# Optimization experiments

Measured on AMD Instinct MI355X. Metric: run time of the kernel, lower is better.

## Reference

```python
import jax, jax.numpy as jnp
import numpy as np

INPUT_SIZE = 256
HIDDEN_SIZE = 1024
NUM_LAYERS = 2
BATCH = 16
SEQ_LEN = 2048
K = 10
JI0 = 0.4
JII = -0.1


def setup_inputs() -> dict:
    key = jax.random.key(0)
    kx, kih, khh, kow, kob = jax.random.split(key, 5)
    x = jax.random.normal(kx, (BATCH, SEQ_LEN, INPUT_SIZE), dtype=jnp.float32)
    # sparse balanced-network init: each entry nonzero with prob K/fan_in, value J/sqrt(K)
    mih = jax.random.bernoulli(kih, K / INPUT_SIZE, (NUM_LAYERS, HIDDEN_SIZE, INPUT_SIZE))
    weight_ih = mih.astype(jnp.float32) * (JI0 / np.sqrt(K))
    mhh = jax.random.bernoulli(khh, K / HIDDEN_SIZE, (NUM_LAYERS, HIDDEN_SIZE, HIDDEN_SIZE))
    weight_hh = mhh.astype(jnp.float32) * (JII / np.sqrt(K))
    out_w = jax.random.normal(kow, (INPUT_SIZE, HIDDEN_SIZE), dtype=jnp.float32) / np.sqrt(HIDDEN_SIZE)
    out_b = jax.random.normal(kob, (INPUT_SIZE,), dtype=jnp.float32) * 0.01
    return {"x": x, "weight_ih": weight_ih, "weight_hh": weight_hh, "out_w": out_w, "out_b": out_b}


def reference(x, weight_ih, weight_hh, out_w, out_b):
    L = weight_hh.shape[0]
    H = weight_hh.shape[1]
    B = x.shape[0]
    c = jnp.sqrt(jnp.asarray(K, dtype=x.dtype))  # const_ff_input (broadcast scalar)
    xs = jnp.transpose(x, (1, 0, 2))  # [S, B, I]  (batch_first -> time major)
    h0 = jnp.zeros((L, B, H), dtype=x.dtype)

    def step(h_prev, x_t):
        hs = []
        for l in range(L):
            if l == 0:
                ff = x_t @ weight_ih[0].T
            else:
                # NOTE: original code uses weight_hh (not weight_ih) for deep-layer ff input
                ff = hs[l - 1] @ weight_hh[l].T
            hs.append(jax.nn.relu(c + ff + h_prev[l] @ weight_hh[l].T))
        h = jnp.stack(hs)  # [L, B, H]
        return h, hs[-1]

    h_T, outs = jax.lax.scan(step, h0, xs)  # outs: [S, B, H]
    out = jnp.transpose(outs, (1, 0, 2)) @ out_w.T + out_b  # [B, S, I]
    return out, h_T
```

## Files before the change

kernel.cpp:

```cpp
#include <hip/hip_runtime.h>
#include <hip/hip_bf16.h>
#include <cstddef>

#define BATCH 16
#define SEQ   2048
#define ISZ   256
#define H     1024
#define CAPE  56
#define MAXDEG 40
#define CAP0  48
#define CAP1  32
#define HP    1056
#define SENTX 256

static __device__ __forceinline__ float bf2f(unsigned short u) {
    unsigned v = ((unsigned)u) << 16;
    float f; __builtin_memcpy(&f, &v, 4); return f;
}


__global__ void init_kernel(unsigned short* eih, unsigned short* e0r, unsigned short* e1r,
                            unsigned short* e0b, unsigned short* e1b,
                            int* cih, int* c0, int* c1, int* sih, int* s0, int* s1,
                            int* nw, float* jv) {
    int t = blockIdx.x * blockDim.x + threadIdx.x;
    if (t < CAPE * H) { eih[t] = SENTX; e0r[t] = 1024; e1r[t] = 1024; e0b[t] = 1024; e1b[t] = 1024; }
    if (t < H) { cih[t] = 0; c0[t] = 0; c1[t] = 0; sih[t] = 0; s0[t] = 0; s1[t] = 0; }
    if (t < 32) nw[t] = 0;
    if (t < 4) jv[t] = 0.f;
}

__global__ void count_ih(const float* __restrict__ wih, int* cih, float* jv) {
    int t = blockIdx.x * blockDim.x + threadIdx.x;
    float w = wih[t];
    if (w != 0.f) { atomicAdd(&cih[t >> 8], 1); jv[0] = w; }
}

__global__ void count_hh(const float* __restrict__ whh, int* c0, int* c1, float* jv) {
    int t = blockIdx.x * blockDim.x + threadIdx.x;
    float w = whh[t];
    if (w != 0.f) {
        int l = t >> 20, j = (t >> 10) & 1023;
        if (l == 0) { atomicAdd(&c0[j], 1); jv[1] = w; }
        else        { atomicAdd(&c1[j], 1); jv[2] = w; }
    }
}

__global__ __launch_bounds__(1024) void sortperm(const int* __restrict__ c0, const int* __restrict__ c1,
                                                 int* p0, int* ip0, int* p1, int* ip1) {
    const int* c = blockIdx.x ? c1 : c0;
    int* p  = blockIdx.x ? p1  : p0;
    int* ip = blockIdx.x ? ip1 : ip0;
    __shared__ int hist[CAPE + 1];
    __shared__ int base[CAPE + 1];
    int j = threadIdx.x;
    if (j <= CAPE) hist[j] = 0;
    __syncthreads();
    int cv = min(c[j], CAPE);
    atomicAdd(&hist[cv], 1);
    __syncthreads();
    if (j == 0) { int acc = 0; for (int k = 0; k <= CAPE; ++k) { base[k] = acc; acc += hist[k]; } }
    __syncthreads();
    int pos = atomicAdd(&base[cv], 1);
    p[pos] = j;
    ip[j] = pos;
}

__global__ void build_ih(const float* __restrict__ wih, const int* __restrict__ ip0,
                         unsigned short* eih, int* sih) {
    int t = blockIdx.x * blockDim.x + threadIdx.x;
    if (wih[t] != 0.f) {
        int j = t >> 8, i = t & 255;
        int r = ip0[j];
        int s = atomicAdd(&sih[r], 1);
        if (s < CAPE) eih[(s >> 1) * (2 * H) + r * 2 + (s & 1)] = (unsigned short)i;
    }
}

__global__ void build_hh(const float* __restrict__ whh, const int* __restrict__ ip0,
                         const int* __restrict__ ip1,
                         unsigned short* e0r, unsigned short* e1r, int* s0, int* s1) {
    int t = blockIdx.x * blockDim.x + threadIdx.x;
    float w = whh[t];
    if (w != 0.f) {
        int l = t >> 20, j = (t >> 10) & 1023, i = t & 1023;
        if (l == 0) {
            int r = ip0[j];
            int s = atomicAdd(&s0[r], 1);
            if (s < CAPE) e0r[(s >> 1) * (2 * H) + r * 2 + (s & 1)] = (unsigned short)ip0[i];
        } else {
            int r = ip1[j];
            int s = atomicAdd(&s1[r], 1);
            if (s < CAPE) e1r[(s >> 1) * (2 * H) + r * 2 + (s & 1)] = (unsigned short)ip1[i];
        }
    }
}

__global__ __launch_bounds__(32) void colorhalf(
    const unsigned short* __restrict__ e0r, const unsigned short* __restrict__ e1r,
    const int* __restrict__ s0, const int* __restrict__ s1,
    unsigned short* e0b, unsigned short* e1b, int* nw)
{
    const int layer = blockIdx.x >> 5;
    const int w = (blockIdx.x >> 1) & 15;
    const int half = blockIdx.x & 1;
    const unsigned short* eraw = layer ? e1r : e0r;
    const int* cnt = layer ? s1 : s0;
    unsigned short* ebal = layer ? e1b : e0b;
    const int cap = layer ? CAP1 : CAP0;

    __shared__ unsigned short lst[32][MAXDEG];
    __shared__ unsigned char colU[32][CAP0];
    __shared__ unsigned char colV[32][CAP0];
    __shared__ unsigned short valU[32][CAP0];
    __shared__ unsigned long long maskU[32], maskV[32];
    __shared__ int deg[32];
    __shared__ int Ss;
    __shared__ unsigned char sentB[CAP0];
    __shared__ unsigned char pu[100], pvv[100], pc[100];
    __shared__ unsigned short pval[100];

    const int lane = threadIdx.x;
    const int r = w * 64 + half * 32 + lane;
    int d = min(cnt[r], MAXDEG);
    deg[lane] = d;
    for (int k = 0; k < d; ++k)
        lst[lane][k] = eraw[(k >> 1) * (2 * H) + r * 2 + (k & 1)];
    for (int c = 0; c < cap; ++c) { colU[lane][c] = 0xFF; colV[lane][c] = 0xFF; }
    __syncthreads();

    if (lane == 0) {
        int bl[32]; for (int b = 0; b < 32; ++b) bl[b] = 0;
        int dmax = 1;
        for (int u = 0; u < 32; ++u) {
            dmax = max(dmax, deg[u]);
            for (int k = 0; k < deg[u]; ++k) bl[lst[u][k] & 31]++;
        }
        int bmax = 0;
        for (int b = 0; b < 32; ++b) bmax = max(bmax, bl[b]);
        int S = max(dmax, bmax); if (S > cap) S = cap; if (S < 8) S = 8;
        Ss = S;
        const unsigned long long full = (1ull << S) - 1ull;
        for (int u = 0; u < 32; ++u) { maskU[u] = full; maskV[u] = full; }

        for (int u = 0; u < 32; ++u) {
            for (int k = 0; k < deg[u]; ++k) {
                const unsigned short val = lst[u][k];
                const int v = val & 31;
                unsigned long long common = maskU[u] & maskV[v];
                if (common) {
                    int c = __ffsll((long long)common) - 1;
                    colU[u][c] = (unsigned char)v; colV[v][c] = (unsigned char)u;
                    valU[u][c] = val;
                    maskU[u] &= ~(1ull << c); maskV[v] &= ~(1ull << c);
                } else {
                    const int a  = __ffsll((long long)maskU[u]) - 1;
                    const int be = __ffsll((long long)maskV[v]) - 1;
                    if (a < 0 || be < 0) {
                        int c = (a >= 0) ? a : ((be >= 0) ? be : 0);
                        colU[u][c] = (unsigned char)v; colV[v][c] = (unsigned char)u;
                        valU[u][c] = val;
                        maskU[u] &= ~(1ull << c); maskV[v] &= ~(1ull << c);
                        continue;
                    }
                    int len = 0, curV = v;
                    for (int g = 0; g < CAP0; ++g) {
                        int uu = colV[curV][a];
                        if (uu == 0xFF) break;
                        pu[len] = (unsigned char)uu; pvv[len] = (unsigned char)curV;
                        pc[len] = (unsigned char)a;  pval[len] = valU[uu][a]; len++;
                        int nv = colU[uu][be];
                        if (nv == 0xFF) break;
                        pu[len] = (unsigned char)uu; pvv[len] = (unsigned char)nv;
                        pc[len] = (unsigned char)be; pval[len] = valU[uu][be]; len++;
                        curV = nv;
                    }
                    for (int i = 0; i < len; ++i) {
                        int uu = pu[i], v2 = pvv[i], c = pc[i];
                        colU[uu][c] = 0xFF; colV[v2][c] = 0xFF;
                        maskU[uu] |= (1ull << c); maskV[v2] |= (1ull << c);
                    }
                    for (int i = 0; i < len; ++i) {
                        int uu = pu[i], v2 = pvv[i];
                        int c2 = (pc[i] == a) ? be : a;
                        colU[uu][c2] = (unsigned char)v2; colV[v2][c2] = (unsigned char)uu;
                        valU[uu][c2] = pval[i];
                        maskU[uu] &= ~(1ull << c2); maskV[v2] &= ~(1ull << c2);
                    }
                    unsigned long long cm = maskU[u] & maskV[v];
                    int c = cm ? (__ffsll((long long)cm) - 1) : a;
                    colU[u][c] = (unsigned char)v; colV[v][c] = (unsigned char)u;
                    valU[u][c] = val;
                    maskU[u] &= ~(1ull << c); maskV[v] &= ~(1ull << c);
                }
            }
        }
    }
    __syncthreads();
    const int S = Ss;
    for (int c = lane; c < cap; c += 32) {
        int bb = c & 31;
        if (c < S) {
            for (int b = 0; b < 32; ++b)
                if ((maskV[b] >> c) & 1) { bb = b; break; }
        }
        sentB[c] = (unsigned char)bb;
    }
    __syncthreads();
    for (int c = 0; c < cap; ++c) {
        unsigned short val = (c < S && colU[lane][c] != 0xFF)
                                 ? valU[lane][c]
                                 : (unsigned short)(1024 + sentB[c]);
        ebal[(c >> 1) * (2 * H) + r * 2 + (c & 1)] = val;
    }
    if (lane == 0) {
        int S8 = (S + 7) & ~7; if (S8 > cap) S8 = cap;
        atomicMax(&nw[layer * 16 + w], S8 >> 3);
    }
}

__global__ void cvt_w(const float* __restrict__ w, const int* __restrict__ p1,
                      __hip_bfloat16* __restrict__ o) {
    int t = blockIdx.x * blockDim.x + threadIdx.x;
    int n = t >> 10, j = t & 1023;
    o[t] = __float2bfloat16(w[n * H + p1[j]]);
}


__global__ __launch_bounds__(256) void ff0_kernel(
    const float* __restrict__ x, const unsigned int* __restrict__ eih,
    const int* __restrict__ cih, const int* __restrict__ p0, const float* __restrict__ jv,
    __hip_bfloat16* __restrict__ ff0) {
    __shared__ float xl[SENTX + 1];
    const int bt = blockIdx.x;
    const int tid = threadIdx.x;
    xl[tid] = x[(size_t)bt * ISZ + tid];
    if (tid == 0) xl[SENTX] = 0.f;
    __syncthreads();
    const float jih = jv[0];
#pragma unroll
    for (int k = 0; k < 4; ++k) {
        const int j = k * 256 + tid;
        const int m = min(cih[p0[j]], CAPE);
        const int nwp = (m + 1) >> 1;
        float s = 0.f;
        for (int w = 0; w < nwp; ++w) {
            unsigned d = eih[w * H + j];
            s += xl[d & 0xffffu] + xl[d >> 16];
        }
        ff0[(size_t)bt * H + j] = __float2bfloat16(jih * s);
    }
}


#define LBAR() asm volatile("s_waitcnt lgkmcnt(0)\n\ts_barrier" ::: "memory")

#define GSUM(PTR, WARR, NG, MAXG, SA, SB, SC, SD)                           \
    _Pragma("unroll")                                                       \
    for (int g = 0; g < (MAXG); ++g) {                                      \
        if (g < (NG)) {                                                     \
            _Pragma("unroll")                                               \
            for (int q = 0; q < 4; ++q) {                                   \
                unsigned wd = (WARR)[g * 4 + q];                            \
                float va = *(const float*)((PTR) + (wd & 0xffffu));         \
                float vb = *(const float*)((PTR) + (wd >> 16));             \
                if (q & 1) { SC += va; SD += vb; }                          \
                else       { SA += va; SB += vb; }                          \
            }                                                               \
        }                                                                   \
    }

#define STEP(PAR, TT) {                                                       \
    unsigned short ffn = fpu[(size_t)((TT) + 1) * H + j];                     \
    const char* h0prev = (const char*)h0b[(PAR) ^ 1];                         \
    const char* uprev  = (const char*)ub[PAR];                                \
    float s0a = 0.f, s0b = 0.f, s0c = 0.f, s0d = 0.f;                         \
    float s1a = 0.f, s1b = 0.f, s1c = 0.f, s1d = 0.f;                         \
    GSUM(h0prev, w0, ng0, 6, s0a, s0b, s0c, s0d)                              \
    GSUM(uprev,  w1, ng1, 4, s1a, s1b, s1c, s1d)                              \
    float h0map = *(const float*)(h0prev + map01b);                           \
    float h0n = fmaxf(bf2f(ffr) + fmaf(jhh0, (s0a + s0c) + (s0b + s0d), cc), 0.f); \
    float h1n = fmaxf(fmaf(jhh1, (s1a + s1c) + (s1b + s1d), cc), 0.f);        \
    if ((TT) < 2) h1n = 0.f;                                                  \
    if ((TT) < SEQ) h0b[PAR][j] = h0n;                                        \
    ub[(PAR) ^ 1][j] = h0map + h1n;                                           \
    if ((TT) >= 2) hp[(size_t)((TT) - 2) * H + j] = __float2bfloat16(h1n);    \
    h1last = h1n;                                                             \
    ffr = ffn;                                                                \
    LBAR();                                                                   \
}

__global__ __launch_bounds__(1024) void rnn_kernel(
    const unsigned short* __restrict__ ff0,
    const unsigned int* __restrict__ ell0, const unsigned int* __restrict__ ell1,
    const int* __restrict__ nwg,
    const int* __restrict__ p0, const int* __restrict__ p1, const int* __restrict__ ip0,
    const float* __restrict__ jv,
    __hip_bfloat16* __restrict__ h1out,
    float* __restrict__ hT)
{
    __shared__ float h0b[2][HP];
    __shared__ float ub[2][HP];

    const int j = threadIdx.x;
    const int b = blockIdx.x;

    h0b[1][j] = 0.f; ub[0][j] = 0.f; ub[1][j] = 0.f;
    if (j < 32) {
        h0b[0][1024 + j] = 0.f; h0b[1][1024 + j] = 0.f;
        ub[0][1024 + j] = 0.f;  ub[1][1024 + j] = 0.f;
    }

    const float jhh0 = jv[1], jhh1 = jv[2];
    const float cc = sqrtf(10.f);
    const int myp1 = p1[j];
    const unsigned map01b = (unsigned)ip0[myp1] * 4u;
    const int w = j >> 6;
    const int ng0 = min(__builtin_amdgcn_readfirstlane(nwg[w]), 6);
    const int ng1 = min(__builtin_amdgcn_readfirstlane(nwg[16 + w]), 4);

    unsigned w0[24], w1[16];
#pragma unroll
    for (int p = 0; p < 24; ++p) {
        unsigned d = ell0[p * H + j];
        w0[p] = ((d & 0xffffu) << 2) | ((d >> 16) << 18);
    }
#pragma unroll
    for (int p = 0; p < 16; ++p) {
        unsigned e = ell1[p * H + j];
        w1[p] = ((e & 0xffffu) << 2) | ((e >> 16) << 18);
    }

    const unsigned short* fpu = ff0 + (size_t)b * SEQ * H;
    __hip_bfloat16* hp = h1out + (size_t)b * SEQ * H;
    unsigned short ffr = fpu[j];
    float h1last = 0.f;

    __syncthreads();

    for (int t = 0; t < SEQ + 2; t += 2) {
        STEP(0, t)
        STEP(1, t + 1)
    }
    hT[(size_t)b * H + p0[j]] = h0b[1][j];
    hT[(size_t)BATCH * H + (size_t)b * H + myp1] = h1last;
}


typedef __attribute__((ext_vector_type(8))) short short8;
typedef __attribute__((ext_vector_type(4))) float f32x4;

__global__ __launch_bounds__(256) void proj_kernel(
    const __hip_bfloat16* __restrict__ h1,
    const __hip_bfloat16* __restrict__ wbf,
    const float* __restrict__ outb,
    float* __restrict__ out)
{
    const int wid  = (blockIdx.x * 256 + threadIdx.x) >> 6;
    const int lane = threadIdx.x & 63;
    const int nb = wid & 3;
    const int mt = wid >> 2;
    const int q  = lane >> 4;
    const int lm = lane & 15;

    const short* A = (const short*)h1 + (size_t)(mt * 16 + lm) * H + q * 8;
    const short* Bbase = (const short*)wbf + q * 8;

    f32x4 acc[4] = {};
#pragma unroll 4
    for (int k = 0; k < H; k += 32) {
        short8 a = *(const short8*)(A + k);
#pragma unroll
        for (int nt = 0; nt < 4; ++nt) {
            const short* Bp = Bbase + (size_t)(nb * 64 + nt * 16 + lm) * H + k;
            short8 bf = *(const short8*)Bp;
            acc[nt] = __builtin_amdgcn_mfma_f32_16x16x32_bf16(a, bf, acc[nt], 0, 0, 0);
        }
    }
#pragma unroll
    for (int nt = 0; nt < 4; ++nt) {
        const int col = nb * 64 + nt * 16 + lm;
        const float bias = outb[col];
#pragma unroll
        for (int r = 0; r < 4; ++r) {
            const int row = mt * 16 + q * 4 + r;
            out[(size_t)row * 256 + col] = acc[nt][r] + bias;
        }
    }
}


extern "C" void kernel_launch(void* const* d_in, const int* in_sizes, int n_in,
                              void* d_out, int out_size, void* d_ws, size_t ws_size,
                              hipStream_t stream) {
    const float* x    = (const float*)d_in[0];
    const float* wih  = (const float*)d_in[1];
    const float* whh  = (const float*)d_in[2];
    const float* outw = (const float*)d_in[3];
    const float* outb = (const float*)d_in[4];
    float* out = (float*)d_out;

    char* ws = (char*)d_ws;
    size_t off = 0;
    __hip_bfloat16* h1buf = (__hip_bfloat16*)(ws + off); off += (size_t)BATCH * SEQ * H * 2;
    __hip_bfloat16* ff0   = (__hip_bfloat16*)(ws + off); off += ((size_t)BATCH * SEQ + 4) * H * 2;
    __hip_bfloat16* wbf   = (__hip_bfloat16*)(ws + off); off += (size_t)ISZ * H * 2;
    unsigned short* eih = (unsigned short*)(ws + off); off += (size_t)CAPE * H * 2;
    unsigned short* e0r = (unsigned short*)(ws + off); off += (size_t)CAPE * H * 2;
    unsigned short* e1r = (unsigned short*)(ws + off); off += (size_t)CAPE * H * 2;
    unsigned short* e0b = (unsigned short*)(ws + off); off += (size_t)CAPE * H * 2;
    unsigned short* e1b = (unsigned short*)(ws + off); off += (size_t)CAPE * H * 2;
    int* cih = (int*)(ws + off); off += (size_t)H * 4;
    int* c0  = (int*)(ws + off); off += (size_t)H * 4;
    int* c1  = (int*)(ws + off); off += (size_t)H * 4;
    int* sih = (int*)(ws + off); off += (size_t)H * 4;
    int* s0  = (int*)(ws + off); off += (size_t)H * 4;
    int* s1  = (int*)(ws + off); off += (size_t)H * 4;
    int* p0  = (int*)(ws + off); off += (size_t)H * 4;
    int* ip0 = (int*)(ws + off); off += (size_t)H * 4;
    int* p1  = (int*)(ws + off); off += (size_t)H * 4;
    int* ip1 = (int*)(ws + off); off += (size_t)H * 4;
    int* nwg = (int*)(ws + off); off += 32 * 4;
    float* jv = (float*)(ws + off); off += 64;
    (void)ws_size; (void)in_sizes; (void)n_in; (void)out_size;

    init_kernel<<<(CAPE * H + 255) / 256, 256, 0, stream>>>(eih, e0r, e1r, e0b, e1b,
                                                            cih, c0, c1, sih, s0, s1, nwg, jv);
    count_ih<<<(H * ISZ) / 256, 256, 0, stream>>>(wih, cih, jv);
    count_hh<<<(2 * H * H) / 256, 256, 0, stream>>>(whh, c0, c1, jv);
    sortperm<<<2, 1024, 0, stream>>>(c0, c1, p0, ip0, p1, ip1);
    build_ih<<<(H * ISZ) / 256, 256, 0, stream>>>(wih, ip0, eih, sih);
    build_hh<<<(2 * H * H) / 256, 256, 0, stream>>>(whh, ip0, ip1, e0r, e1r, s0, s1);
    colorhalf<<<64, 32, 0, stream>>>(e0r, e1r, s0, s1, e0b, e1b, nwg);
    cvt_w<<<(ISZ * H) / 256, 256, 0, stream>>>(outw, p1, wbf);
    ff0_kernel<<<BATCH * SEQ, 256, 0, stream>>>(x, (const unsigned int*)eih, cih, p0, jv, ff0);

    float* hT = out + (size_t)BATCH * SEQ * ISZ;
    rnn_kernel<<<BATCH, 1024, 0, stream>>>((const unsigned short*)ff0,
                                           (const unsigned int*)e0b, (const unsigned int*)e1b,
                                           nwg, p0, p1, ip0, jv, h1buf, hT);
    proj_kernel<<<2048, 256, 0, stream>>>(h1buf, wbf, outb, out);
}
```

Baseline: 2.585 ms.

## Duplicate recurrent state into a bank-permuted LDS copy to balance gather banks

Each hidden-state and update value is now written twice to LDS: once at its natural index and once in a second half at a bank-permuted position (XOR with the upper index bits). The edge-coloring preprocessing can then pick, for each sparse edge, whichever of the two copies lands in the less loaded bank, and encodes that choice in the gather index. The goal is to cut the per-step colour count, and with it the LDS bank conflicts and gather rounds in the recurrent loop. The cost is doubled LDS footprint, an extra LDS store per state element per step, and sentinel indices moved to 2048.

```diff
diff --git a/kernel.cpp b/kernel.cpp
--- a/kernel.cpp
+++ b/kernel.cpp
@@ -10,7 +10,7 @@
 #define MAXDEG 40
 #define CAP0  48
 #define CAP1  32
-#define HP    1056
+#define HB    2080
 #define SENTX 256
 
 static __device__ __forceinline__ float bf2f(unsigned short u) {
@@ -24,7 +24,7 @@
                             int* cih, int* c0, int* c1, int* sih, int* s0, int* s1,
                             int* nw, float* jv) {
     int t = blockIdx.x * blockDim.x + threadIdx.x;
-    if (t < CAPE * H) { eih[t] = SENTX; e0r[t] = 1024; e1r[t] = 1024; e0b[t] = 1024; e1b[t] = 1024; }
+    if (t < CAPE * H) { eih[t] = SENTX; e0r[t] = 1024; e1r[t] = 1024; e0b[t] = 2048; e1b[t] = 2048; }
     if (t < H) { cih[t] = 0; c0[t] = 0; c1[t] = 0; sih[t] = 0; s0[t] = 0; s1[t] = 0; }
     if (t < 32) nw[t] = 0;
     if (t < 4) jv[t] = 0.f;
@@ -110,6 +110,8 @@
     const int cap = layer ? CAP1 : CAP0;
 
     __shared__ unsigned short lst[32][MAXDEG];
+    __shared__ unsigned short encS[32][MAXDEG];
+    __shared__ unsigned char bnk[32][MAXDEG];
     __shared__ unsigned char colU[32][CAP0];
     __shared__ unsigned char colV[32][CAP0];
     __shared__ unsigned short valU[32][CAP0];
@@ -132,9 +134,19 @@
     if (lane == 0) {
         int bl[32]; for (int b = 0; b < 32; ++b) bl[b] = 0;
         int dmax = 1;
+        for (int u = 0; u < 32; ++u) dmax = max(dmax, deg[u]);
         for (int u = 0; u < 32; ++u) {
-            dmax = max(dmax, deg[u]);
-            for (int k = 0; k < deg[u]; ++k) bl[lst[u][k] & 31]++;
+            for (int k = 0; k < deg[u]; ++k) {
+                int idx = lst[u][k];
+                int bA = idx & 31;
+                int bB = (idx ^ (idx >> 5)) & 31;
+                int useB = bl[bB] < bl[bA];
+                int cb = useB ? bB : bA;
+                bl[cb]++;
+                bnk[u][k] = (unsigned char)cb;
+                encS[u][k] = useB ? (unsigned short)(1024 + ((idx & ~31) | bB))
+                                  : (unsigned short)idx;
+            }
         }
         int bmax = 0;
         for (int b = 0; b < 32; ++b) bmax = max(bmax, bl[b]);
@@ -145,8 +157,8 @@
 
         for (int u = 0; u < 32; ++u) {
             for (int k = 0; k < deg[u]; ++k) {
-                const unsigned short val = lst[u][k];
-                const int v = val & 31;
+                const unsigned short val = encS[u][k];
+                const int v = bnk[u][k];
                 unsigned long long common = maskU[u] & maskV[v];
                 if (common) {
                     int c = __ffsll((long long)common) - 1;
@@ -210,7 +222,7 @@
     for (int c = 0; c < cap; ++c) {
         unsigned short val = (c < S && colU[lane][c] != 0xFF)
                                  ? valU[lane][c]
-                                 : (unsigned short)(1024 + sentB[c]);
+                                 : (unsigned short)(2048 + sentB[c]);
         ebal[(c >> 1) * (2 * H) + r * 2 + (c & 1)] = val;
     }
     if (lane == 0) {
@@ -282,8 +294,9 @@
     float h0n = fmaxf(bf2f(ffr) + fmaf(jhh0, (s0a + s0c) + (s0b + s0d), cc), 0.f); \
     float h1n = fmaxf(fmaf(jhh1, (s1a + s1c) + (s1b + s1d), cc), 0.f);        \
     if ((TT) < 2) h1n = 0.f;                                                  \
-    if ((TT) < SEQ) h0b[PAR][j] = h0n;                                        \
-    ub[(PAR) ^ 1][j] = h0map + h1n;                                           \
+    if ((TT) < SEQ) { h0b[PAR][j] = h0n; h0b[PAR][1024 + pj] = h0n; }         \
+    float un = h0map + h1n;                                                   \
+    ub[(PAR) ^ 1][j] = un; ub[(PAR) ^ 1][1024 + pj] = un;                     \
     if ((TT) >= 2) hp[(size_t)((TT) - 2) * H + j] = __float2bfloat16(h1n);    \
     h1last = h1n;                                                             \
     ffr = ffn;                                                                \
@@ -299,22 +312,25 @@
     __hip_bfloat16* __restrict__ h1out,
     float* __restrict__ hT)
 {
-    __shared__ float h0b[2][HP];
-    __shared__ float ub[2][HP];
+    __shared__ float h0b[2][HB];
+    __shared__ float ub[2][HB];
 
     const int j = threadIdx.x;
     const int b = blockIdx.x;
 
-    h0b[1][j] = 0.f; ub[0][j] = 0.f; ub[1][j] = 0.f;
+    h0b[1][j] = 0.f; h0b[1][1024 + j] = 0.f;
+    ub[0][j] = 0.f;  ub[0][1024 + j] = 0.f;
+    ub[1][j] = 0.f;  ub[1][1024 + j] = 0.f;
     if (j < 32) {
-        h0b[0][1024 + j] = 0.f; h0b[1][1024 + j] = 0.f;
-        ub[0][1024 + j] = 0.f;  ub[1][1024 + j] = 0.f;
+        h0b[0][2048 + j] = 0.f; h0b[1][2048 + j] = 0.f;
+        ub[0][2048 + j] = 0.f;  ub[1][2048 + j] = 0.f;
     }
 
     const float jhh0 = jv[1], jhh1 = jv[2];
     const float cc = sqrtf(10.f);
     const int myp1 = p1[j];
     const unsigned map01b = (unsigned)ip0[myp1] * 4u;
+    const int pj = (j & ~31) | ((j ^ (j >> 5)) & 31);
     const int w = j >> 6;
     const int ng0 = min(__builtin_amdgcn_readfirstlane(nwg[w]), 6);
     const int ng1 = min(__builtin_amdgcn_readfirstlane(nwg[16 + w]), 4);
```

After: 2.405 ms. 7.0% less time.
